# Kernel optimization log

Hardware: AMD Instinct MI355X
Metric: run time of the kernel (lower is better)

## Reference

```python
import functools
import jax, jax.numpy as jnp
import numpy as np

N = 8192
CUTOFF = 0.125        # OpenBoundary._cutoff
INCLUDE_SELF = False  # OpenBoundary._include_self
MASK_VALUE = -1


def setup_inputs() -> dict:
    key = jax.random.key(0)
    positions = jax.random.uniform(key, (N, 3), dtype=jnp.float32)
    return {"positions": positions, "max_neighbours": 128}


def reference(positions, max_neighbours):
    n = positions.shape[0]
    c2 = CUTOFF * CUTOFF
    # all-pairs squared distances + cutoff mask; row i = sphere centred on particle i
    neigh_mask = jax.vmap(lambda c: jnp.sum((positions - c) ** 2, axis=1) <= c2)(positions)  # [N, N] bool
    if not INCLUDE_SELF:
        neigh_mask = neigh_mask & ~jnp.eye(n, dtype=bool)
    # per-row fixed-size compaction of true indices, padded with MASK_VALUE
    compact = functools.partial(jnp.argwhere, size=max_neighbours, fill_value=MASK_VALUE)
    to_idx = jax.vmap(compact)(neigh_mask)[..., 0]                 # [N, max_neighbours] int
    cell_indices = jnp.zeros((*to_idx.shape, 3), dtype=jnp.int32)  # open boundary: all zero cells
    actual_max_neighbours = jnp.max(neigh_mask.sum(axis=1))
    return to_idx, cell_indices, actual_max_neighbours
```

## Files before the change

kernel.cpp:

```cpp
#include <hip/hip_runtime.h>
#include <stdint.h>


#define CUTOFF2 (0.125f * 0.125f)
constexpr int NCELLS = 512;
constexpr int CAP    = 64;
constexpr int MAXN   = 128;
constexpr int NPART  = 256;
constexpr int CANDMAX = 27 * CAP;

__device__ __forceinline__ int ccoord(float v) {
    int c = (int)(v * 8.0f);
    return c > 7 ? 7 : c;
}

__global__ __launch_bounds__(256) void scatter_kernel(
    const float* __restrict__ pos, int n,
    int* __restrict__ cnt, float4* __restrict__ cells) {
    int i = blockIdx.x * blockDim.x + threadIdx.x;
    if (i >= n) return;
    float x = pos[i*3], y = pos[i*3+1], z = pos[i*3+2];
    int c = (ccoord(z) * 8 + ccoord(y)) * 8 + ccoord(x);
    int slot = atomicAdd(&cnt[c], 1);
    cells[c * CAP + slot] = make_float4(x, y, z, __int_as_float(i));
}

__global__ __launch_bounds__(512) void neigh_kernel(
    const float4* __restrict__ cells,
    const int* __restrict__ cnt,
    int maxn,
    int* __restrict__ to_idx,
    int* __restrict__ cell_out,
    int* __restrict__ partial) {
    __shared__ float4   cand[CANDMAX];
    __shared__ uint32_t bm[8][256];
    __shared__ int scid[27], scnt[27], soff[28];

    const int tid  = threadIdx.x;
    const int lane = tid & 63;
    const int wave = tid >> 6;
    const int cell = blockIdx.x;
    const int cx = cell & 7, cy = (cell >> 3) & 7, cz = cell >> 6;

    if (tid < 64) {
        int dzz = tid / 9 - 1, dyy = (tid / 3) % 3 - 1, dxx = tid % 3 - 1;
        int xx = cx + dxx, yy = cy + dyy, zz = cz + dzz;
        bool ok = (tid < 27) & ((unsigned)xx <= 7u) &
                  ((unsigned)yy <= 7u) & ((unsigned)zz <= 7u);
        int c = (zz * 8 + yy) * 8 + xx;
        int v = ok ? cnt[c] : 0;
        if (tid < 27) { scid[tid] = ok ? c : -1; scnt[tid] = v; }
        int incl = v;
        #pragma unroll
        for (int d = 1; d < 32; d <<= 1) {
            int o = __shfl_up(incl, d);
            if (lane >= d) incl += o;
        }
        if (tid < 27) soff[tid + 1] = incl;
        if (tid == 0) soff[0] = 0;
    }
    __syncthreads();

    const int mrows = scnt[13];
    const int cbase = soff[13];
    if (mrows == 0) return;

    for (int j = wave; j < 27; j += 8) {
        int c = scid[j];
        if (c >= 0 && lane < scnt[j])
            cand[soff[j] + lane] = cells[c * CAP + lane];
    }
    __syncthreads();

    const int T = soff[27];
    uint32_t* mybm = bm[wave];

    for (int r = wave; r < mrows; r += 8) {
        float4 me = cand[cbase + r];
        const int row = __float_as_int(me.w);

        ((int4*)mybm)[lane] = make_int4(0, 0, 0, 0);

        int4* co = (int4*)(cell_out + (size_t)row * maxn * 3);
        co[lane] = make_int4(0, 0, 0, 0);
        if (lane < 32) co[64 + lane] = make_int4(0, 0, 0, 0);

        int s = lane;
        for (; s + 64 < T; s += 128) {
            float4 q0 = cand[s];
            float4 q1 = cand[s + 64];
            float dx0 = q0.x - me.x, dy0 = q0.y - me.y, dz0 = q0.z - me.z;
            float dx1 = q1.x - me.x, dy1 = q1.y - me.y, dz1 = q1.z - me.z;
            float d20 = dx0*dx0 + dy0*dy0 + dz0*dz0;
            float d21 = dx1*dx1 + dy1*dy1 + dz1*dz1;
            int i0 = __float_as_int(q0.w);
            int i1 = __float_as_int(q1.w);
            if (d20 <= CUTOFF2 && i0 != row)
                atomicOr(&mybm[i0 >> 5], 1u << (i0 & 31));
            if (d21 <= CUTOFF2 && i1 != row)
                atomicOr(&mybm[i1 >> 5], 1u << (i1 & 31));
        }
        if (s < T) {
            float4 q = cand[s];
            float ddx = q.x - me.x, ddy = q.y - me.y, ddz = q.z - me.z;
            float d2 = ddx*ddx + ddy*ddy + ddz*ddz;
            int i0 = __float_as_int(q.w);
            if (d2 <= CUTOFF2 && i0 != row)
                atomicOr(&mybm[i0 >> 5], 1u << (i0 & 31));
        }

        int4 wv = ((int4*)mybm)[lane];
        uint32_t w0 = (uint32_t)wv.x, w1 = (uint32_t)wv.y,
                 w2 = (uint32_t)wv.z, w3 = (uint32_t)wv.w;
        int tc = __popc(w0) + __popc(w1) + __popc(w2) + __popc(w3);

        int inc = tc;
        #pragma unroll
        for (int d = 1; d < 64; d <<= 1) {
            int o = __shfl_up(inc, d);
            if (lane >= d) inc += o;
        }
        const int total = __shfl(inc, 63);
        int p = inc - tc;

        int* out_row = to_idx + (size_t)row * maxn;
        const int bitbase = lane << 7;
        uint32_t wsv[4] = {w0, w1, w2, w3};
        #pragma unroll
        for (int d = 0; d < 4; ++d) {
            uint32_t mm = wsv[d];
            while (mm) {
                int b = __ffs(mm) - 1;
                if (p < MAXN) out_row[p] = bitbase + (d << 5) + b;
                ++p;
                mm &= mm - 1;
            }
        }
        int start = total < MAXN ? total : MAXN;
        for (int q = start + lane; q < MAXN; q += 64) out_row[q] = -1;

        if (lane == 0) atomicMax(&partial[blockIdx.x & (NPART - 1)], total);
    }
}

__global__ __launch_bounds__(256) void maxred_kernel(
    const int* __restrict__ partial, int* __restrict__ out_max) {
    __shared__ int sm[4];
    int m = partial[threadIdx.x];
    #pragma unroll
    for (int d = 32; d > 0; d >>= 1) {
        int o = __shfl_down(m, d);
        m = o > m ? o : m;
    }
    if ((threadIdx.x & 63) == 0) sm[threadIdx.x >> 6] = m;
    __syncthreads();
    if (threadIdx.x == 0) {
        int r = sm[0];
        r = sm[1] > r ? sm[1] : r;
        r = sm[2] > r ? sm[2] : r;
        *out_max = r > sm[3] ? r : sm[3];
    }
}

extern "C" void kernel_launch(void* const* d_in, const int* in_sizes, int n_in,
                              void* d_out, int out_size, void* d_ws, size_t ws_size,
                              hipStream_t stream) {
    const float* pos = (const float*)d_in[0];
    const int n = in_sizes[0] / 3;
    const int maxn = (out_size - 1) / (n * 4);

    int* to_idx   = (int*)d_out;
    int* cell_out = to_idx + (size_t)n * maxn;
    int* out_max  = cell_out + (size_t)n * maxn * 3;

    int*    cnt     = (int*)d_ws;
    int*    partial = cnt + NCELLS;
    float4* cells   = (float4*)((char*)d_ws + 4096);

    hipMemsetAsync(d_ws, 0, (NCELLS + NPART) * sizeof(int), stream);
    scatter_kernel<<<(n + 255) / 256, 256, 0, stream>>>(pos, n, cnt, cells);
    neigh_kernel<<<NCELLS, 512, 0, stream>>>(cells, cnt, maxn,
                                             to_idx, cell_out, partial);
    maxred_kernel<<<1, NPART, 0, stream>>>(partial, out_max);
}
```

Measured before the change: 84.07 us.

## Fuse scatter, neighbour search and max reduction into one kernel with grid barrier

Merges the three kernels (cell scatter, neighbour compaction, max reduction) into one persistent launch of 512 blocks. A software grid-wide barrier on an atomic counter separates the scatter phase from the neighbour phase. The per-block max is reduced in shared memory and then pushed with a single global atomic max, replacing the partial array and the separate reduction kernel. This removes two kernel launches and their gaps. In exchange it depends on all 512 blocks being co-resident, which the launch bounds are meant to allow; if they are not, the barrier deadlocks.

```diff
diff --git a/kernel.cpp b/kernel.cpp
--- a/kernel.cpp
+++ b/kernel.cpp
@@ -3,10 +3,9 @@
 
 
 #define CUTOFF2 (0.125f * 0.125f)
-constexpr int NCELLS = 512;
-constexpr int CAP    = 64;
-constexpr int MAXN   = 128;
-constexpr int NPART  = 256;
+constexpr int NCELLS  = 512;
+constexpr int CAP     = 64;
+constexpr int MAXN    = 128;
 constexpr int CANDMAX = 27 * CAP;
 
 __device__ __forceinline__ int ccoord(float v) {
@@ -14,32 +13,52 @@
     return c > 7 ? 7 : c;
 }
 
-__global__ __launch_bounds__(256) void scatter_kernel(
-    const float* __restrict__ pos, int n,
-    int* __restrict__ cnt, float4* __restrict__ cells) {
-    int i = blockIdx.x * blockDim.x + threadIdx.x;
-    if (i >= n) return;
-    float x = pos[i*3], y = pos[i*3+1], z = pos[i*3+2];
-    int c = (ccoord(z) * 8 + ccoord(y)) * 8 + ccoord(x);
-    int slot = atomicAdd(&cnt[c], 1);
-    cells[c * CAP + slot] = make_float4(x, y, z, __int_as_float(i));
+__device__ __forceinline__ void grid_barrier(int* bar, int nblocks) {
+    __syncthreads();
+    if (threadIdx.x == 0) {
+        __threadfence();
+        __hip_atomic_fetch_add(bar, 1, __ATOMIC_ACQ_REL, __HIP_MEMORY_SCOPE_AGENT);
+        while (__hip_atomic_load(bar, __ATOMIC_ACQUIRE, __HIP_MEMORY_SCOPE_AGENT)
+               < nblocks) {
+            __builtin_amdgcn_s_sleep(8);
+        }
+        __threadfence();
+    }
+    __syncthreads();
 }
 
-__global__ __launch_bounds__(512) void neigh_kernel(
-    const float4* __restrict__ cells,
-    const int* __restrict__ cnt,
-    int maxn,
+__global__ __launch_bounds__(512, 4) void fused_kernel(
+    const float* __restrict__ pos, int n, int maxn,
     int* __restrict__ to_idx,
     int* __restrict__ cell_out,
-    int* __restrict__ partial) {
+    int* __restrict__ out_max,
+    int* __restrict__ cnt,
+    int* __restrict__ bar,
+    float4* __restrict__ cells)
+{
     __shared__ float4   cand[CANDMAX];
     __shared__ uint32_t bm[8][256];
     __shared__ int scid[27], scnt[27], soff[28];
+    __shared__ int blkmax;
 
     const int tid  = threadIdx.x;
     const int lane = tid & 63;
     const int wave = tid >> 6;
     const int cell = blockIdx.x;
+
+    {
+        const int i = cell * 512 + tid;
+        if (i < n) {
+            float x = pos[i*3], y = pos[i*3+1], z = pos[i*3+2];
+            int c = (ccoord(z) * 8 + ccoord(y)) * 8 + ccoord(x);
+            int slot = atomicAdd(&cnt[c], 1);
+            cells[c * CAP + slot] = make_float4(x, y, z, __int_as_float(i));
+        }
+        if (cell == 0 && tid == 0) *out_max = 0;
+    }
+
+    grid_barrier(bar, NCELLS);
+
     const int cx = cell & 7, cy = (cell >> 3) & 7, cz = cell >> 6;
 
     if (tid < 64) {
@@ -57,7 +76,7 @@
             if (lane >= d) incl += o;
         }
         if (tid < 27) soff[tid + 1] = incl;
-        if (tid == 0) soff[0] = 0;
+        if (tid == 0) { soff[0] = 0; blkmax = 0; }
     }
     __syncthreads();
 
@@ -139,47 +158,31 @@
         int start = total < MAXN ? total : MAXN;
         for (int q = start + lane; q < MAXN; q += 64) out_row[q] = -1;
 
-        if (lane == 0) atomicMax(&partial[blockIdx.x & (NPART - 1)], total);
+        if (lane == 0) atomicMax(&blkmax, total);
     }
-}
 
-__global__ __launch_bounds__(256) void maxred_kernel(
-    const int* __restrict__ partial, int* __restrict__ out_max) {
-    __shared__ int sm[4];
-    int m = partial[threadIdx.x];
-    #pragma unroll
-    for (int d = 32; d > 0; d >>= 1) {
-        int o = __shfl_down(m, d);
-        m = o > m ? o : m;
-    }
-    if ((threadIdx.x & 63) == 0) sm[threadIdx.x >> 6] = m;
     __syncthreads();
-    if (threadIdx.x == 0) {
-        int r = sm[0];
-        r = sm[1] > r ? sm[1] : r;
-        r = sm[2] > r ? sm[2] : r;
-        *out_max = r > sm[3] ? r : sm[3];
-    }
+    if (tid == 0 && blkmax > 0)
+        __hip_atomic_fetch_max(out_max, blkmax, __ATOMIC_RELAXED,
+                               __HIP_MEMORY_SCOPE_AGENT);
 }
 
 extern "C" void kernel_launch(void* const* d_in, const int* in_sizes, int n_in,
                               void* d_out, int out_size, void* d_ws, size_t ws_size,
                               hipStream_t stream) {
     const float* pos = (const float*)d_in[0];
-    const int n = in_sizes[0] / 3;
-    const int maxn = (out_size - 1) / (n * 4);
+    int n = in_sizes[0] / 3;
+    int maxn = (out_size - 1) / (n * 4);
 
     int* to_idx   = (int*)d_out;
     int* cell_out = to_idx + (size_t)n * maxn;
     int* out_max  = cell_out + (size_t)n * maxn * 3;
 
-    int*    cnt     = (int*)d_ws;
-    int*    partial = cnt + NCELLS;
-    float4* cells   = (float4*)((char*)d_ws + 4096);
+    int*    cnt   = (int*)d_ws;
+    int*    bar   = cnt + NCELLS;
+    float4* cells = (float4*)((char*)d_ws + 4096);
 
-    hipMemsetAsync(d_ws, 0, (NCELLS + NPART) * sizeof(int), stream);
-    scatter_kernel<<<(n + 255) / 256, 256, 0, stream>>>(pos, n, cnt, cells);
-    neigh_kernel<<<NCELLS, 512, 0, stream>>>(cells, cnt, maxn,
-                                             to_idx, cell_out, partial);
-    maxred_kernel<<<1, NPART, 0, stream>>>(partial, out_max);
+    hipMemsetAsync(d_ws, 0, (NCELLS + 1) * sizeof(int), stream);
+    fused_kernel<<<NCELLS, 512, 0, stream>>>(pos, n, maxn, to_idx, cell_out,
+                                             out_max, cnt, bar, cells);
 }
```

Measured after the change: 119.9 us. 42.6% more time.
